# Kernel optimization log

Hardware: AMD Instinct MI355X
Metric: run time of the kernel (lower is better)

Reference implementation:

```python
import jax, jax.numpy as jnp
import numpy as np

HEADS = 16
EMBED = 1024
HEAD_DIM = EMBED // HEADS


def setup_inputs() -> dict:
    key = jax.random.key(0)
    ks = jax.random.split(key, 10)
    B, SQ, SKV = 2, 2048, 2048
    s = 1.0 / np.sqrt(HEAD_DIM)
    sd = 1.0 / np.sqrt(EMBED)
    return {
        "queries": jax.random.normal(ks[0], (B, SQ, EMBED), jnp.float32),
        "values": jax.random.normal(ks[1], (B, SKV, EMBED), jnp.float32),
        "heads": HEADS,
        "Wv": jax.random.normal(ks[2], (HEAD_DIM, HEAD_DIM), jnp.float32) * s,
        "bv": jax.random.normal(ks[3], (HEAD_DIM,), jnp.float32) * 0.02,
        "Wk": jax.random.normal(ks[4], (HEAD_DIM, HEAD_DIM), jnp.float32) * s,
        "bk": jax.random.normal(ks[5], (HEAD_DIM,), jnp.float32) * 0.02,
        "Wq": jax.random.normal(ks[6], (HEAD_DIM, HEAD_DIM), jnp.float32) * s,
        "bq": jax.random.normal(ks[7], (HEAD_DIM,), jnp.float32) * 0.02,
        "Wd": jax.random.normal(ks[8], (EMBED, EMBED), jnp.float32) * sd,
        "bd": jax.random.normal(ks[9], (EMBED,), jnp.float32) * 0.02,
    }


def reference(queries, values, heads, Wv, bv, Wk, bk, Wq, bq, Wd, bd):
    n, sq, e = queries.shape
    skv = values.shape[1]
    d = e // heads
    # reshape to per-head layout [b, s, h, d]
    q_in = queries.reshape(n, sq, heads, d)
    v_in = values.reshape(n, skv, heads, d)
    # shared per-head linear projections (torch Linear: x @ W.T + b)
    v = jnp.einsum("bshd,ed->bshe", v_in, Wv) + bv
    # quirk preserved: keys computed from the ALREADY-PROJECTED values
    k = jnp.einsum("bshd,ed->bshe", v, Wk) + bk
    q = jnp.einsum("bshd,ed->bshe", q_in, Wq) + bq
    # full O(n^2) score matrix [b, h, sq, skv] (as in source)
    scores = jnp.einsum("bqhd,bkhd->bhqk", q, k) / jnp.sqrt(jnp.asarray(d, q.dtype))
    attn = jax.nn.softmax(scores, axis=-1)
    out = jnp.einsum("bhqk,bkhd->bqhd", attn, v).reshape(n, sq, e)
    return out @ Wd.T + bd
```

## Files before the change

kernel.cpp:

```cpp
#include <hip/hip_runtime.h>
#include <hip/hip_bf16.h>
#include <hip/hip_fp16.h>
#include <math.h>

typedef _Float16 f16;
typedef _Float16 f16x8 __attribute__((ext_vector_type(8)));
typedef _Float16 f16x4 __attribute__((ext_vector_type(4)));
typedef _Float16 f16x2 __attribute__((ext_vector_type(2)));
typedef unsigned short u16x8v __attribute__((ext_vector_type(8)));
typedef float f32x4 __attribute__((ext_vector_type(4)));

namespace {
constexpr int B = 2;
constexpr int H = 16;
constexpr int S = 2048;
constexpr int D = 64;
constexpr int E = 1024;
constexpr float QSCALE = 0.125f * 1.4426950408889634f;
}

#define GLOBAL_LOAD_LDS16(gp, lp)                                              \
  __builtin_amdgcn_global_load_lds(                                            \
      (const __attribute__((address_space(1))) void*)(gp),                     \
      (__attribute__((address_space(3))) void*)(lp), 16, 0, 0)

__global__ __launch_bounds__(256) void prep(const float* __restrict__ Wd, f16* __restrict__ wd16,
                                            const float* __restrict__ Wk, const float* __restrict__ Wv,
                                            const float* __restrict__ bv, const float* __restrict__ bk,
                                            float* __restrict__ Wkv, float* __restrict__ bkv) {
  if (blockIdx.x < 1024) {
    const int i = blockIdx.x * 256 + threadIdx.x;
    const float4 f = ((const float4*)Wd)[i];
    f16x4 o;
    o.x = (f16)f.x; o.y = (f16)f.y; o.z = (f16)f.z; o.w = (f16)f.w;
    *(f16x4*)(wd16 + 4 * (size_t)i) = o;
  } else {
    const int g = (blockIdx.x - 1024) * 256 + threadIdx.x;
    const int i = g >> 6, j = g & 63;
    float s = 0.f;
#pragma unroll 16
    for (int d = 0; d < 64; ++d) s = fmaf(Wk[i * 64 + d], Wv[d * 64 + j], s);
    Wkv[g] = s;
    if (g < 64) {
      float bb = bk[g];
#pragma unroll 16
      for (int d = 0; d < 64; ++d) bb = fmaf(Wk[g * 64 + d], bv[d], bb);
      bkv[g] = bb;
    }
  }
}

__global__ __launch_bounds__(256) void proj3_mfma(const float* __restrict__ xq,
                                                  const float* __restrict__ xv,
                                                  const float* __restrict__ Wq,
                                                  const float* __restrict__ bq,
                                                  const float* __restrict__ Wv,
                                                  const float* __restrict__ bv,
                                                  const float* __restrict__ Wkv,
                                                  const float* __restrict__ bkv,
                                                  f16* __restrict__ qp,
                                                  f16* __restrict__ vtp,
                                                  f16* __restrict__ kp) {
  __shared__ f16 tb[16 * 16 * 64];
  const int which = blockIdx.y;
  const float* x = which ? xv : xq;

  const int t = threadIdx.x, lane = t & 63, w = t >> 6;
  const int l15 = lane & 15, quad = lane >> 4;
  const int m0 = (blockIdx.x * 4 + w) * 64;

  f16x8 af[4][2];
#pragma unroll
  for (int mt = 0; mt < 4; ++mt)
#pragma unroll
    for (int kc = 0; kc < 2; ++kc) {
      const float* g = x + (size_t)(m0 + mt * 16 + l15) * 64 + kc * 32 + quad * 8;
      const float4 a = *(const float4*)g, b2 = *(const float4*)(g + 4);
      f16x8 v;
      v[0]=(f16)a.x; v[1]=(f16)a.y; v[2]=(f16)a.z; v[3]=(f16)a.w;
      v[4]=(f16)b2.x; v[5]=(f16)b2.y; v[6]=(f16)b2.z; v[7]=(f16)b2.w;
      af[mt][kc] = v;
    }

  const int npass = which ? 2 : 1;
  for (int pass = 0; pass < npass; ++pass) {
    const float* W    = which ? (pass ? Wkv : Wv) : Wq;
    const float* bias = which ? (pass ? bkv : bv) : bq;
    const bool vpass  = (which == 1) && (pass == 0);
    f16* out          = which ? (pass ? kp : (f16*)nullptr) : qp;
    const float scale = which ? 1.0f : QSCALE;

    f16x8 wf[4][2];
#pragma unroll
    for (int nt = 0; nt < 4; ++nt)
#pragma unroll
      for (int kc = 0; kc < 2; ++kc) {
        const float* g = W + (size_t)(nt * 16 + l15) * 64 + kc * 32 + quad * 8;
        const float4 a = *(const float4*)g, b2 = *(const float4*)(g + 4);
        f16x8 v;
        v[0]=(f16)a.x; v[1]=(f16)a.y; v[2]=(f16)a.z; v[3]=(f16)a.w;
        v[4]=(f16)b2.x; v[5]=(f16)b2.y; v[6]=(f16)b2.z; v[7]=(f16)b2.w;
        wf[nt][kc] = v;
      }

    f32x4 acc[4][4];
#pragma unroll
    for (int nt = 0; nt < 4; ++nt)
#pragma unroll
      for (int mt = 0; mt < 4; ++mt) acc[nt][mt] = (f32x4){0.f, 0.f, 0.f, 0.f};
#pragma unroll
    for (int kc = 0; kc < 2; ++kc)
#pragma unroll
      for (int nt = 0; nt < 4; ++nt)
#pragma unroll
        for (int mt = 0; mt < 4; ++mt)
          acc[nt][mt] = __builtin_amdgcn_mfma_f32_16x16x32_f16(wf[nt][kc], af[mt][kc], acc[nt][mt], 0, 0, 0);

    float4 bl4[4];
#pragma unroll
    for (int nt = 0; nt < 4; ++nt) bl4[nt] = *(const float4*)&bias[nt * 16 + quad * 4];

#pragma unroll
    for (int mt = 0; mt < 4; ++mt) {
      const int g = m0 + mt * 16 + l15;
      const int h = g & 15, bs_ = g >> 4;
      const int b = bs_ >> 11, s = bs_ & 2047;
      f16* o = vpass ? nullptr : (out + ((size_t)(b * H + h) * S + s) * 64 + quad * 4);
#pragma unroll
      for (int nt = 0; nt < 4; ++nt) {
        const float p0 = (acc[nt][mt][0] + bl4[nt].x) * scale;
        const float p1 = (acc[nt][mt][1] + bl4[nt].y) * scale;
        const float p2 = (acc[nt][mt][2] + bl4[nt].z) * scale;
        const float p3 = (acc[nt][mt][3] + bl4[nt].w) * scale;
        union { f16x4 v4; f16x2 hh[2]; } u;
        u.hh[0] = __builtin_bit_cast(f16x2, __builtin_amdgcn_cvt_pkrtz(p0, p1));
        u.hh[1] = __builtin_bit_cast(f16x2, __builtin_amdgcn_cvt_pkrtz(p2, p3));
        if (vpass) {
#pragma unroll
          for (int r = 0; r < 4; ++r)
            tb[(l15 * 64 + nt * 16 + quad * 4 + r) * 16 + w * 4 + mt] = u.v4[r];
        } else {
          *(f16x4*)(o + nt * 16) = u.v4;
        }
      }
    }

    if (vpass) {
      __syncthreads();
      const int bsb = blockIdx.x * 16;
      const int bb = bsb >> 11;
      const int sb = bsb & 2047;
      const int off = sb & 63;
      const int poff = (off & 32) | ((off & 16) >> 2);
      const int col0 = (sb - off) + poff;
#pragma unroll
      for (int k2 = 0; k2 < 4; ++k2) {
        const int pi = t * 4 + k2;
        const int h = pi >> 6, d = pi & 63;
        const f16x8 lo = *(const f16x8*)&tb[pi * 16];
        const f16x8 hi = *(const f16x8*)&tb[pi * 16 + 8];
        f16* orow = vtp + ((size_t)(bb * H + h) * 64 + d) * S + col0;
        f16x4 g0, g1, g2, g3;
#pragma unroll
        for (int j = 0; j < 4; ++j) { g0[j]=lo[j]; g1[j]=lo[4+j]; g2[j]=hi[j]; g3[j]=hi[4+j]; }
        *(f16x4*)(orow + 0)  = g0;
        *(f16x4*)(orow + 8)  = g1;
        *(f16x4*)(orow + 16) = g2;
        *(f16x4*)(orow + 24) = g3;
      }
      __syncthreads();
    }
  }
}

__global__ __launch_bounds__(256) void attn_mfma(const f16* __restrict__ qp,
                                                 const f16* __restrict__ kp,
                                                 const f16* __restrict__ vtp,
                                                 f16* __restrict__ ao) {
  __shared__ f16 ks[4][64 * 64];
  __shared__ f16 vs[4][64 * 64];
  const int t = threadIdx.x, lane = t & 63, w = t >> 6;
  const int l15 = lane & 15, quad = lane >> 4;
  const int bh = blockIdx.x;
  const int q0 = blockIdx.y * 128;
  const f16* qbase = qp + ((size_t)bh * S + q0 + w * 32) * D;
  const f16* kbase = kp + (size_t)bh * S * D;
  const f16* vtbase = vtp + (size_t)bh * 64 * S;

  const int c1 = w * 64 + lane;
  const int row1 = c1 >> 3;
  const int sc1 = (c1 & 7) ^ (row1 & 7);
  const size_t koff1 = (size_t)row1 * D + sc1 * 8;
  const size_t koff2 = koff1 + (size_t)32 * D;
  const size_t voff1 = (size_t)row1 * S + sc1 * 8;
  const size_t voff2 = voff1 + (size_t)32 * S;

  f16x8 qf[2][2];
#pragma unroll
  for (int mt = 0; mt < 2; ++mt)
#pragma unroll
    for (int kc = 0; kc < 2; ++kc)
      qf[mt][kc] = *(const f16x8*)(qbase + (size_t)(mt * 16 + l15) * D + kc * 32 + quad * 8);

  f16x8 vb4;
#pragma unroll
  for (int j = 0; j < 8; ++j) vb4[j] = (l15 == 0) ? (f16)1.0f : (f16)0.0f;

  f32x4 O[2][5];
#pragma unroll
  for (int mt = 0; mt < 2; ++mt)
#pragma unroll
    for (int nt = 0; nt < 5; ++nt) O[mt][nt] = (f32x4){0.f, 0.f, 0.f, 0.f};

#define ISSUE_TILE(tt, buf)                                                    \
  {                                                                            \
    const f16* gk = kbase + (size_t)(tt) * (64 * D);                           \
    GLOBAL_LOAD_LDS16(gk + koff1, &ks[buf][w * 512]);                          \
    GLOBAL_LOAD_LDS16(gk + koff2, &ks[buf][2048 + w * 512]);                   \
    const f16* gv = vtbase + (size_t)(tt) * 64;                                \
    GLOBAL_LOAD_LDS16(gv + voff1, &vs[buf][w * 512]);                          \
    GLOBAL_LOAD_LDS16(gv + voff2, &vs[buf][2048 + w * 512]);                   \
  }

  int kofs[4][2];
#pragma unroll
  for (int nt = 0; nt < 4; ++nt)
#pragma unroll
    for (int kc = 0; kc < 2; ++kc)
      kofs[nt][kc] = (nt * 16 + l15) * 64 + (((kc * 4 + quad) ^ (l15 & 7)) * 8);

  f16x8 kfA[4][2], kfB[4][2];

  ISSUE_TILE(0, 0);
  ISSUE_TILE(1, 1);
  __asm__ volatile("s_waitcnt vmcnt(4)" ::: "memory");
  __builtin_amdgcn_s_barrier();
  __asm__ volatile("" ::: "memory");
#pragma unroll
  for (int nt = 0; nt < 4; ++nt)
#pragma unroll
    for (int kc = 0; kc < 2; ++kc) kfA[nt][kc] = *(const f16x8*)&ks[0][kofs[nt][kc]];

  auto STEP = [&](int kt, f16x8 (&kfc)[4][2], f16x8 (&kfn)[4][2]) {
    {
      const int tt = (kt + 2 < S / 64) ? (kt + 2) : (S / 64 - 1);
      ISSUE_TILE(tt, (kt + 2) & 3);
    }

    f32x4 sc[4][2];
#pragma unroll
    for (int nt = 0; nt < 4; ++nt)
#pragma unroll
      for (int mt = 0; mt < 2; ++mt) sc[nt][mt] = (f32x4){0.f, 0.f, 0.f, 0.f};
    __builtin_amdgcn_s_setprio(1);
#pragma unroll
    for (int kc = 0; kc < 2; ++kc)
#pragma unroll
      for (int nt = 0; nt < 4; ++nt)
#pragma unroll
        for (int mt = 0; mt < 2; ++mt)
          sc[nt][mt] = __builtin_amdgcn_mfma_f32_16x16x32_f16(kfc[nt][kc], qf[mt][kc], sc[nt][mt], 0, 0, 0);
    __builtin_amdgcn_s_setprio(0);

    f16x8 pa[2][2];
#pragma unroll
    for (int mt = 0; mt < 2; ++mt)
#pragma unroll
      for (int kc = 0; kc < 2; ++kc) {
        const f32x4 s0 = sc[2 * kc][mt], s1 = sc[2 * kc + 1][mt];
        union { f16x8 v8; f16x2 h[4]; } u;
        u.h[0] = __builtin_bit_cast(f16x2, __builtin_amdgcn_cvt_pkrtz(
            __builtin_amdgcn_exp2f(s0[0]), __builtin_amdgcn_exp2f(s0[1])));
        u.h[1] = __builtin_bit_cast(f16x2, __builtin_amdgcn_cvt_pkrtz(
            __builtin_amdgcn_exp2f(s0[2]), __builtin_amdgcn_exp2f(s0[3])));
        u.h[2] = __builtin_bit_cast(f16x2, __builtin_amdgcn_cvt_pkrtz(
            __builtin_amdgcn_exp2f(s1[0]), __builtin_amdgcn_exp2f(s1[1])));
        u.h[3] = __builtin_bit_cast(f16x2, __builtin_amdgcn_cvt_pkrtz(
            __builtin_amdgcn_exp2f(s1[2]), __builtin_amdgcn_exp2f(s1[3])));
        pa[mt][kc] = u.v8;
      }

    __asm__ volatile("s_waitcnt vmcnt(4)" ::: "memory");
    {
      const f16* kb1 = &ks[(kt + 1) & 3][0];
#pragma unroll
      for (int nt = 0; nt < 4; ++nt)
#pragma unroll
        for (int kc = 0; kc < 2; ++kc) kfn[nt][kc] = *(const f16x8*)(kb1 + kofs[nt][kc]);
    }

    __builtin_amdgcn_s_setprio(1);
    const f16* vbuf = &vs[kt & 3][0];
#pragma unroll
    for (int kc = 0; kc < 2; ++kc) {
#pragma unroll
      for (int nt = 0; nt < 4; ++nt) {
        const f16x8 vbf = *(const f16x8*)(vbuf + kofs[nt][kc]);
#pragma unroll
        for (int mt = 0; mt < 2; ++mt)
          O[mt][nt] = __builtin_amdgcn_mfma_f32_16x16x32_f16(pa[mt][kc], vbf, O[mt][nt], 0, 0, 0);
      }
#pragma unroll
      for (int mt = 0; mt < 2; ++mt)
        O[mt][4] = __builtin_amdgcn_mfma_f32_16x16x32_f16(pa[mt][kc], vb4, O[mt][4], 0, 0, 0);
    }
    __builtin_amdgcn_s_setprio(0);

    __builtin_amdgcn_s_barrier();
    __asm__ volatile("" ::: "memory");
  };

  for (int kt2 = 0; kt2 < S / 64; kt2 += 2) {
    STEP(kt2 + 0, kfA, kfB);
    STEP(kt2 + 1, kfB, kfA);
  }
#undef ISSUE_TILE

  const int b = bh >> 4, h = bh & 15;
#pragma unroll
  for (int mt = 0; mt < 2; ++mt)
#pragma unroll
    for (int r = 0; r < 4; ++r) {
      const float l = __shfl(O[mt][4][r], quad << 4, 64);
      const float inv = 1.f / l;
      const int row = q0 + w * 32 + mt * 16 + quad * 4 + r;
      f16* o = ao + ((size_t)b * S + row) * E + h * D;
#pragma unroll
      for (int nt = 0; nt < 4; ++nt)
        o[nt * 16 + l15] = (f16)(O[mt][nt][r] * inv);
    }
}

__global__ __launch_bounds__(256) void dense_mfma(const f16* __restrict__ A,
                                                  const f16* __restrict__ Wd16,
                                                  const float* __restrict__ bd,
                                                  float* __restrict__ out) {
  __shared__ f16 as[3][128 * 64];
  __shared__ f16 bs[3][64 * 64];
  const int t = threadIdx.x;
  const int lane = t & 63;
  const int w = t >> 6;
  const int l15 = lane & 15;
  const int quad = lane >> 4;
  const int m0 = blockIdx.x * 128;
  const int n0 = blockIdx.y * 64;
  const int wm = (w >> 1) * 64, wn = (w & 1) * 32;

  const int srow = (lane >> 3);
  const int schunk = (lane & 7) ^ srow;
  const f16* ga0 = A    + (size_t)(m0 + w * 32 + srow) * E + schunk * 8;
  const f16* gb0 = Wd16 + (size_t)(n0 + w * 16 + srow) * E + schunk * 8;

  constexpr int NT = E / 64;

#define ISSUE_D(tt, ib)                                                        \
  {                                                                            \
    _Pragma("unroll")                                                          \
    for (int i = 0; i < 4; ++i)                                                \
      GLOBAL_LOAD_LDS16(ga0 + (size_t)(i * 8) * E + (tt) * 64,                 \
                        &as[ib][(w * 32 + i * 8) * 64]);                       \
    _Pragma("unroll")                                                          \
    for (int i = 0; i < 2; ++i)                                                \
      GLOBAL_LOAD_LDS16(gb0 + (size_t)(i * 8) * E + (tt) * 64,                 \
                        &bs[ib][(w * 16 + i * 8) * 64]);                       \
  }

  f32x4 acc[4][2];
#pragma unroll
  for (int mt = 0; mt < 4; ++mt)
#pragma unroll
    for (int nt = 0; nt < 2; ++nt) acc[mt][nt] = (f32x4){0.f, 0.f, 0.f, 0.f};

  ISSUE_D(0, 0);
  ISSUE_D(1, 1);
  __asm__ volatile("s_waitcnt vmcnt(6)" ::: "memory");
  __builtin_amdgcn_s_barrier();
  __asm__ volatile("" ::: "memory");

  int rb = 0, ib = 2;
  for (int kt = 0; kt < NT; ++kt) {
    {
      const int tt = (kt + 2 < NT) ? (kt + 2) : (NT - 1);
      ISSUE_D(tt, ib);
    }
    f16x8 af[4][2];
#pragma unroll
    for (int mt = 0; mt < 4; ++mt)
#pragma unroll
      for (int kc = 0; kc < 2; ++kc)
        af[mt][kc] = *(const f16x8*)&as[rb][(wm + mt * 16 + l15) * 64 + (((kc * 4 + quad) ^ (l15 & 7)) * 8)];
#pragma unroll
    for (int kc = 0; kc < 2; ++kc)
#pragma unroll
      for (int nt = 0; nt < 2; ++nt) {
        const f16x8 bf = *(const f16x8*)&bs[rb][(wn + nt * 16 + l15) * 64 + (((kc * 4 + quad) ^ (l15 & 7)) * 8)];
#pragma unroll
        for (int mt = 0; mt < 4; ++mt)
          acc[mt][nt] = __builtin_amdgcn_mfma_f32_16x16x32_f16(af[mt][kc], bf, acc[mt][nt], 0, 0, 0);
      }
    __asm__ volatile("s_waitcnt vmcnt(6)" ::: "memory");
    __builtin_amdgcn_s_barrier();
    __asm__ volatile("" ::: "memory");
    rb = (rb + 1 >= 3) ? 0 : rb + 1;
    ib = (ib + 1 >= 3) ? 0 : ib + 1;
  }
#undef ISSUE_D

#pragma unroll
  for (int nt = 0; nt < 2; ++nt) {
    const int col = n0 + wn + nt * 16 + l15;
    const float bdv = bd[col];
#pragma unroll
    for (int mt = 0; mt < 4; ++mt)
#pragma unroll
      for (int r = 0; r < 4; ++r)
        out[(size_t)(m0 + wm + mt * 16 + quad * 4 + r) * E + col] = acc[mt][nt][r] + bdv;
  }
}

extern "C" void kernel_launch(void* const* d_in, const int* in_sizes, int n_in,
                              void* d_out, int out_size, void* d_ws, size_t ws_size,
                              hipStream_t stream) {
  const float* queries = (const float*)d_in[0];
  const float* values  = (const float*)d_in[1];
  const float* Wv = (const float*)d_in[3];
  const float* bv = (const float*)d_in[4];
  const float* Wk = (const float*)d_in[5];
  const float* bk = (const float*)d_in[6];
  const float* Wq = (const float*)d_in[7];
  const float* bq = (const float*)d_in[8];
  const float* Wd = (const float*)d_in[9];
  const float* bd = (const float*)d_in[10];
  float* out = (float*)d_out;

  char* ws = (char*)d_ws;
  f16* qp    = (f16*)(ws);
  f16* kp    = (f16*)(ws + 8u * 1024 * 1024);
  f16* vtp   = (f16*)(ws + 16u * 1024 * 1024);
  f16* ao    = (f16*)(ws + 24u * 1024 * 1024);
  f16* wd16  = (f16*)(ws + 32u * 1024 * 1024);
  float* wkv = (float*)(ws + 34u * 1024 * 1024);
  float* bkv = (float*)(ws + 34u * 1024 * 1024 + 16384);
  (void)ws_size; (void)in_sizes; (void)n_in; (void)out_size;

  prep<<<1040, 256, 0, stream>>>(Wd, wd16, Wk, Wv, bv, bk, wkv, bkv);
  proj3_mfma<<<dim3(256, 2), 256, 0, stream>>>(queries, values, Wq, bq, Wv, bv, wkv, bkv, qp, vtp, kp);
  attn_mfma<<<dim3(B * H, S / 128), 256, 0, stream>>>(qp, kp, vtp, ao);
  dense_mfma<<<dim3(B * S / 128, E / 64), 256, 0, stream>>>(ao, wd16, bd, out);
}
```

Before: 175.5 us.

## Use 128-key double-buffered attention tiles and stage K output through LDS

The attention loop moves from a 4-deep ring of 64-key tiles with register-prefetched K fragments to a 2-buffer scheme of 128-key tiles. Each tile is followed by a full vmcnt(0) wait and a barrier, and K fragments are read from LDS just before use. Q is now written in the natural [b,s,h,d] layout and read strided by the attention kernel. K is staged through a padded LDS buffer so it can be stored to global memory as contiguous 16-byte rows. Larger tiles halve the number of barriers, but the pipeline becomes shallower and loads may stall more, while the Q reads are no longer contiguous.

```diff
diff --git a/kernel.cpp b/kernel.cpp
--- a/kernel.cpp
+++ b/kernel.cpp
@@ -61,7 +61,7 @@
                                                   f16* __restrict__ qp,
                                                   f16* __restrict__ vtp,
                                                   f16* __restrict__ kp) {
-  __shared__ f16 tb[16 * 16 * 64];
+  __shared__ f16 tb[16 * 16 * 68];
   const int which = blockIdx.y;
   const float* x = which ? xv : xq;
 
@@ -87,7 +87,7 @@
     const float* W    = which ? (pass ? Wkv : Wv) : Wq;
     const float* bias = which ? (pass ? bkv : bv) : bq;
     const bool vpass  = (which == 1) && (pass == 0);
-    f16* out          = which ? (pass ? kp : (f16*)nullptr) : qp;
+    const bool kpass  = (which == 1) && (pass == 1);
     const float scale = which ? 1.0f : QSCALE;
 
     f16x8 wf[4][2];
@@ -123,9 +123,6 @@
 #pragma unroll
     for (int mt = 0; mt < 4; ++mt) {
       const int g = m0 + mt * 16 + l15;
-      const int h = g & 15, bs_ = g >> 4;
-      const int b = bs_ >> 11, s = bs_ & 2047;
-      f16* o = vpass ? nullptr : (out + ((size_t)(b * H + h) * S + s) * 64 + quad * 4);
 #pragma unroll
       for (int nt = 0; nt < 4; ++nt) {
         const float p0 = (acc[nt][mt][0] + bl4[nt].x) * scale;
@@ -139,8 +136,10 @@
 #pragma unroll
           for (int r = 0; r < 4; ++r)
             tb[(l15 * 64 + nt * 16 + quad * 4 + r) * 16 + w * 4 + mt] = u.v4[r];
+        } else if (kpass) {
+          *(f16x4*)&tb[(l15 * 16 + w * 4 + mt) * 68 + nt * 16 + quad * 4] = u.v4;
         } else {
-          *(f16x4*)(o + nt * 16) = u.v4;
+          *(f16x4*)(qp + (size_t)g * 64 + nt * 16 + quad * 4) = u.v4;
         }
       }
     }
@@ -169,6 +168,17 @@
         *(f16x4*)(orow + 24) = g3;
       }
       __syncthreads();
+    } else if (kpass) {
+      __syncthreads();
+      const int bsb = blockIdx.x * 16;
+      const int bb = bsb >> 11;
+      const int sblk = bsb & 2047;
+      const int h = t >> 4, sl = t & 15;
+      f16* dst = kp + ((size_t)(bb * H + h) * S + sblk + sl) * 64;
+      const f16* src = &tb[t * 68];
+#pragma unroll
+      for (int c = 0; c < 8; ++c)
+        *(f16x8*)(dst + c * 8) = *(const f16x8*)(src + c * 8);
     }
   }
 }
@@ -177,30 +187,29 @@
                                                  const f16* __restrict__ kp,
                                                  const f16* __restrict__ vtp,
                                                  f16* __restrict__ ao) {
-  __shared__ f16 ks[4][64 * 64];
-  __shared__ f16 vs[4][64 * 64];
+  __shared__ f16 ks[2][128 * 64];
+  __shared__ f16 vs[2][64 * 128];
   const int t = threadIdx.x, lane = t & 63, w = t >> 6;
   const int l15 = lane & 15, quad = lane >> 4;
   const int bh = blockIdx.x;
+  const int b = bh >> 4, h = bh & 15;
   const int q0 = blockIdx.y * 128;
-  const f16* qbase = qp + ((size_t)bh * S + q0 + w * 32) * D;
   const f16* kbase = kp + (size_t)bh * S * D;
   const f16* vtbase = vtp + (size_t)bh * 64 * S;
 
   const int c1 = w * 64 + lane;
-  const int row1 = c1 >> 3;
-  const int sc1 = (c1 & 7) ^ (row1 & 7);
-  const size_t koff1 = (size_t)row1 * D + sc1 * 8;
-  const size_t koff2 = koff1 + (size_t)32 * D;
-  const size_t voff1 = (size_t)row1 * S + sc1 * 8;
-  const size_t voff2 = voff1 + (size_t)32 * S;
+  const int krow = c1 >> 3;
+  const size_t koff1 = (size_t)krow * D + (((c1 & 7) ^ (krow & 7)) * 8);
+  const int vrow = c1 >> 4;
+  const size_t voff1 = (size_t)vrow * S + (((c1 & 15) ^ (vrow & 7)) * 8);
 
   f16x8 qf[2][2];
 #pragma unroll
   for (int mt = 0; mt < 2; ++mt)
 #pragma unroll
     for (int kc = 0; kc < 2; ++kc)
-      qf[mt][kc] = *(const f16x8*)(qbase + (size_t)(mt * 16 + l15) * D + kc * 32 + quad * 8);
+      qf[mt][kc] = *(const f16x8*)(qp +
+          ((size_t)(b * S + q0 + w * 32 + mt * 16 + l15) * H + h) * 64 + kc * 32 + quad * 8);
 
   f16x8 vb4;
 #pragma unroll
@@ -214,88 +223,68 @@
 
 #define ISSUE_TILE(tt, buf)                                                    \
   {                                                                            \
-    const f16* gk = kbase + (size_t)(tt) * (64 * D);                           \
-    GLOBAL_LOAD_LDS16(gk + koff1, &ks[buf][w * 512]);                          \
-    GLOBAL_LOAD_LDS16(gk + koff2, &ks[buf][2048 + w * 512]);                   \
-    const f16* gv = vtbase + (size_t)(tt) * 64;                                \
-    GLOBAL_LOAD_LDS16(gv + voff1, &vs[buf][w * 512]);                          \
-    GLOBAL_LOAD_LDS16(gv + voff2, &vs[buf][2048 + w * 512]);                   \
-  }
-
-  int kofs[4][2];
-#pragma unroll
-  for (int nt = 0; nt < 4; ++nt)
-#pragma unroll
-    for (int kc = 0; kc < 2; ++kc)
-      kofs[nt][kc] = (nt * 16 + l15) * 64 + (((kc * 4 + quad) ^ (l15 & 7)) * 8);
-
-  f16x8 kfA[4][2], kfB[4][2];
+    const f16* gk = kbase + (size_t)(tt) * (128 * D);                          \
+    _Pragma("unroll")                                                          \
+    for (int i = 0; i < 4; ++i)                                                \
+      GLOBAL_LOAD_LDS16(gk + koff1 + (size_t)i * (32 * D),                     \
+                        &ks[buf][(i * 256 + w * 64) * 8]);                     \
+    const f16* gv = vtbase + (size_t)(tt) * 128;                               \
+    _Pragma("unroll")                                                          \
+    for (int i = 0; i < 4; ++i)                                                \
+      GLOBAL_LOAD_LDS16(gv + voff1 + (size_t)i * (16 * S),                     \
+                        &vs[buf][(i * 256 + w * 64) * 8]);                     \
+  }
 
   ISSUE_TILE(0, 0);
-  ISSUE_TILE(1, 1);
-  __asm__ volatile("s_waitcnt vmcnt(4)" ::: "memory");
-  __builtin_amdgcn_s_barrier();
-  __asm__ volatile("" ::: "memory");
-#pragma unroll
-  for (int nt = 0; nt < 4; ++nt)
-#pragma unroll
-    for (int kc = 0; kc < 2; ++kc) kfA[nt][kc] = *(const f16x8*)&ks[0][kofs[nt][kc]];
-
-  auto STEP = [&](int kt, f16x8 (&kfc)[4][2], f16x8 (&kfn)[4][2]) {
-    {
-      const int tt = (kt + 2 < S / 64) ? (kt + 2) : (S / 64 - 1);
-      ISSUE_TILE(tt, (kt + 2) & 3);
-    }
-
-    f32x4 sc[4][2];
-#pragma unroll
-    for (int nt = 0; nt < 4; ++nt)
+
+  for (int kt = 0; kt < S / 128; ++kt) {
+    const int rb = kt & 1;
+    __asm__ volatile("s_waitcnt vmcnt(0)" ::: "memory");
+    __builtin_amdgcn_s_barrier();
+    __asm__ volatile("" ::: "memory");
+    if (kt + 1 < S / 128) ISSUE_TILE(kt + 1, rb ^ 1);
+
+    f32x4 sc[8][2];
+#pragma unroll
+    for (int nt = 0; nt < 8; ++nt)
 #pragma unroll
       for (int mt = 0; mt < 2; ++mt) sc[nt][mt] = (f32x4){0.f, 0.f, 0.f, 0.f};
     __builtin_amdgcn_s_setprio(1);
 #pragma unroll
     for (int kc = 0; kc < 2; ++kc)
 #pragma unroll
-      for (int nt = 0; nt < 4; ++nt)
+      for (int nt = 0; nt < 8; ++nt) {
+        const f16x8 kf = *(const f16x8*)&ks[rb][(nt * 16 + l15) * 64 + (((kc * 4 + quad) ^ (l15 & 7)) * 8)];
 #pragma unroll
         for (int mt = 0; mt < 2; ++mt)
-          sc[nt][mt] = __builtin_amdgcn_mfma_f32_16x16x32_f16(kfc[nt][kc], qf[mt][kc], sc[nt][mt], 0, 0, 0);
+          sc[nt][mt] = __builtin_amdgcn_mfma_f32_16x16x32_f16(kf, qf[mt][kc], sc[nt][mt], 0, 0, 0);
+      }
     __builtin_amdgcn_s_setprio(0);
 
-    f16x8 pa[2][2];
+    f16x8 pa[2][4];
 #pragma unroll
     for (int mt = 0; mt < 2; ++mt)
 #pragma unroll
-      for (int kc = 0; kc < 2; ++kc) {
+      for (int kc = 0; kc < 4; ++kc) {
         const f32x4 s0 = sc[2 * kc][mt], s1 = sc[2 * kc + 1][mt];
-        union { f16x8 v8; f16x2 h[4]; } u;
-        u.h[0] = __builtin_bit_cast(f16x2, __builtin_amdgcn_cvt_pkrtz(
+        union { f16x8 v8; f16x2 hh[4]; } u;
+        u.hh[0] = __builtin_bit_cast(f16x2, __builtin_amdgcn_cvt_pkrtz(
             __builtin_amdgcn_exp2f(s0[0]), __builtin_amdgcn_exp2f(s0[1])));
-        u.h[1] = __builtin_bit_cast(f16x2, __builtin_amdgcn_cvt_pkrtz(
+        u.hh[1] = __builtin_bit_cast(f16x2, __builtin_amdgcn_cvt_pkrtz(
             __builtin_amdgcn_exp2f(s0[2]), __builtin_amdgcn_exp2f(s0[3])));
-        u.h[2] = __builtin_bit_cast(f16x2, __builtin_amdgcn_cvt_pkrtz(
+        u.hh[2] = __builtin_bit_cast(f16x2, __builtin_amdgcn_cvt_pkrtz(
             __builtin_amdgcn_exp2f(s1[0]), __builtin_amdgcn_exp2f(s1[1])));
-        u.h[3] = __builtin_bit_cast(f16x2, __builtin_amdgcn_cvt_pkrtz(
+        u.hh[3] = __builtin_bit_cast(f16x2, __builtin_amdgcn_cvt_pkrtz(
             __builtin_amdgcn_exp2f(s1[2]), __builtin_amdgcn_exp2f(s1[3])));
         pa[mt][kc] = u.v8;
       }
 
-    __asm__ volatile("s_waitcnt vmcnt(4)" ::: "memory");
-    {
-      const f16* kb1 = &ks[(kt + 1) & 3][0];
-#pragma unroll
-      for (int nt = 0; nt < 4; ++nt)
-#pragma unroll
-        for (int kc = 0; kc < 2; ++kc) kfn[nt][kc] = *(const f16x8*)(kb1 + kofs[nt][kc]);
-    }
-
     __builtin_amdgcn_s_setprio(1);
-    const f16* vbuf = &vs[kt & 3][0];
-#pragma unroll
-    for (int kc = 0; kc < 2; ++kc) {
+#pragma unroll
+    for (int kc = 0; kc < 4; ++kc) {
 #pragma unroll
       for (int nt = 0; nt < 4; ++nt) {
-        const f16x8 vbf = *(const f16x8*)(vbuf + kofs[nt][kc]);
+        const f16x8 vbf = *(const f16x8*)&vs[rb][(nt * 16 + l15) * 128 + (((kc * 4 + quad) ^ (l15 & 7)) * 8)];
 #pragma unroll
         for (int mt = 0; mt < 2; ++mt)
           O[mt][nt] = __builtin_amdgcn_mfma_f32_16x16x32_f16(pa[mt][kc], vbf, O[mt][nt], 0, 0, 0);
@@ -305,18 +294,9 @@
         O[mt][4] = __builtin_amdgcn_mfma_f32_16x16x32_f16(pa[mt][kc], vb4, O[mt][4], 0, 0, 0);
     }
     __builtin_amdgcn_s_setprio(0);
-
-    __builtin_amdgcn_s_barrier();
-    __asm__ volatile("" ::: "memory");
-  };
-
-  for (int kt2 = 0; kt2 < S / 64; kt2 += 2) {
-    STEP(kt2 + 0, kfA, kfB);
-    STEP(kt2 + 1, kfB, kfA);
   }
 #undef ISSUE_TILE
 
-  const int b = bh >> 4, h = bh & 15;
 #pragma unroll
   for (int mt = 0; mt < 2; ++mt)
 #pragma unroll
```

New measurement: 177.7 us. About the same (+1.3%).
